# Kernel tuning notes

Measured on AMD Instinct MI355X. Metric: run time of the kernel, lower is better.

## Reference

```python
import jax, jax.numpy as jnp
import numpy as np

EPS = 1e-5

def _layernorm(x, g, b):
    # normalize over last (channel) axis
    mu = jnp.mean(x, axis=-1, keepdims=True)
    var = jnp.var(x, axis=-1, keepdims=True)
    return (x - mu) * jax.lax.rsqrt(var + EPS) * g + b

def _dynamix(xt, wnd, bnd, wnn, bnn):
    # xt: [B, M, N, C]; mixes over the N axis (vectorized form of the per-slice loop)
    B, M, N, C = xt.shape
    d = wnd.shape[1]
    p = xt @ wnd + bnd                       # [B,M,N,d]
    p = p.reshape(B, M, N * d) @ wnn + bnn   # [B,M,N*N]
    p = jax.nn.softmax(p.reshape(B, M, N, N), axis=-1)
    return jnp.einsum('bmij,bmjc->bmic', p, xt)  # [B,M,N,C]

def setup_inputs() -> dict:
    key = jax.random.key(0)
    ks = jax.random.split(key, 10)
    B, C, H, W, d, E = 32, 128, 56, 56, 10, 4
    def n(k, shape, scale=0.02):
        return jax.random.normal(k, shape, jnp.float32) * scale
    return {
        'x': jax.random.normal(ks[0], (B, C, H, W), jnp.float32),
        'ln1_g': jnp.ones((C,), jnp.float32), 'ln1_b': jnp.zeros((C,), jnp.float32),
        'h_wnd': n(ks[1], (C, d)), 'h_bnd': jnp.zeros((d,), jnp.float32),
        'h_wnn': n(ks[2], (W * d, W * W)), 'h_bnn': jnp.zeros((W * W,), jnp.float32),
        'w_wnd': n(ks[3], (C, d)), 'w_bnd': jnp.zeros((d,), jnp.float32),
        'w_wnn': n(ks[4], (H * d, H * H)), 'w_bnn': jnp.zeros((H * H,), jnp.float32),
        'pc_w': n(ks[5], (C, C)), 'pc_b': jnp.zeros((C,), jnp.float32),
        'po_w': n(ks[6], (C, C)), 'po_b': jnp.zeros((C,), jnp.float32),
        'ln2_g': jnp.ones((C,), jnp.float32), 'ln2_b': jnp.zeros((C,), jnp.float32),
        'fc1_w': n(ks[7], (C, E * C)), 'fc1_b': jnp.zeros((E * C,), jnp.float32),
        'fc2_w': n(ks[8], (E * C, C)), 'fc2_b': jnp.zeros((C,), jnp.float32),
    }

def reference(x, ln1_g, ln1_b, h_wnd, h_bnd, h_wnn, h_bnn,
              w_wnd, w_bnd, w_wnn, w_bnn, pc_w, pc_b, po_w, po_b,
              ln2_g, ln2_b, fc1_w, fc1_b, fc2_w, fc2_b):
    # x: [B,C,H,W] -> work channels-last [B,H,W,C]
    xt = jnp.transpose(x, (0, 2, 3, 1))
    # ---- block p1: LN + DynaMixer ----
    u = _layernorm(xt, ln1_g, ln1_b)                 # [B,H,W,C]
    y_h = _dynamix(u, h_wnd, h_bnd, h_wnn, h_bnn)    # mix over W per row
    u_w = jnp.transpose(u, (0, 2, 1, 3))             # [B,W,H,C]
    y_w = _dynamix(u_w, w_wnd, w_bnd, w_wnn, w_bnn)  # mix over H per col
    y_w = jnp.transpose(y_w, (0, 2, 1, 3))           # back to [B,H,W,C]
    y_c = u @ pc_w + pc_b                            # 1x1 conv proj_c
    y = (y_h + y_w + y_c) @ po_w + po_b              # 1x1 conv proj_o
    xt = xt + y                                      # residual (drop_path=0)
    # ---- block p2: LN + MLP ----
    v = _layernorm(xt, ln2_g, ln2_b)
    h = jax.nn.gelu(v @ fc1_w + fc1_b, approximate=False)
    h = h @ fc2_w + fc2_b
    xt = xt + h
    return jnp.transpose(xt, (0, 3, 1, 2))           # [B,C,H,W]
```

## Files before the change

kernel.cpp:

```cpp
#include <hip/hip_runtime.h>
#include <math.h>

#define BB 32
#define CC 128
#define HH 56
#define WW 56
#define HWHW 3136
#define TOK 100352
#define BH 1792
#define NDP 576
#define NNP 3200

typedef __attribute__((ext_vector_type(8))) short bhalf8;
typedef __attribute__((ext_vector_type(4))) float f32x4;
typedef __attribute__((ext_vector_type(4))) unsigned int u32x4;

__device__ inline unsigned short f2bf(float f) {
  unsigned int x = __float_as_uint(f);
  unsigned int r = (x + 0x7FFFu + ((x >> 16) & 1u)) >> 16;
  return (unsigned short)r;
}
__device__ inline float bf2f(unsigned short u) {
  return __uint_as_float(((unsigned int)u) << 16);
}
__device__ inline unsigned int pack2(float a, float b) {
  return (unsigned int)f2bf(a) | ((unsigned int)f2bf(b) << 16);
}
__device__ inline f32x4 MFMA(bhalf8 a, bhalf8 b, f32x4 c) {
  return __builtin_amdgcn_mfma_f32_16x16x32_bf16(a, b, c, 0, 0, 0);
}
template <int CH>
__device__ inline bhalf8 ldsFrag(const unsigned short* base, int row, int chunk) {
  return *reinterpret_cast<const bhalf8*>(base + row * (CH * 8) + ((chunk ^ (row & 7)) * 8));
}
__device__ inline float gelu_f(float x) {
  float x3 = x * x * x;
  float z = 0.7978845608028654f * (x + 0.044715f * x3);
  float e = __expf(2.0f * z);
  float t = 1.0f - 2.0f / (e + 1.0f);
  return 0.5f * x * (1.0f + t);
}

__global__ __launch_bounds__(256) void wcvt_kernel(
    const float* __restrict__ hwnn, const float* __restrict__ wwnn,
    const float* __restrict__ pcw, const float* __restrict__ pow_,
    const float* __restrict__ fc1w, const float* __restrict__ fc2w,
    const float* __restrict__ hwnd, const float* __restrict__ wwnd,
    unsigned short* __restrict__ wnnTh, unsigned short* __restrict__ wnnTw,
    unsigned short* __restrict__ pcT, unsigned short* __restrict__ poT,
    unsigned short* __restrict__ fc1T, unsigned short* __restrict__ fc2T,
    unsigned short* __restrict__ wcatT, u32x4* __restrict__ pdzero) {
  int gt = blockIdx.x * 256 + threadIdx.x;
  int gs = gridDim.x * 256;
  for (int i = gt; i < 258048; i += gs) { u32x4 z = {0, 0, 0, 0}; pdzero[i] = z; }
  for (int i = gt; i < 3200 * 576; i += gs) {
    int k = i / 3200, n = i % 3200;
    float v = (n < 3136 && k < 560) ? hwnn[(size_t)k * 3136 + n] : 0.f;
    wnnTh[(size_t)n * 576 + k] = f2bf(v);
  }
  for (int i = gt; i < 3200 * 576; i += gs) {
    int k = i / 3200, n = i % 3200;
    float v = (n < 3136 && k < 560) ? wwnn[(size_t)k * 3136 + n] : 0.f;
    wnnTw[(size_t)n * 576 + k] = f2bf(v);
  }
  for (int i = gt; i < 128 * 128; i += gs) { int k = i >> 7, n = i & 127; pcT[n * 128 + k] = f2bf(pcw[i]); }
  for (int i = gt; i < 128 * 128; i += gs) { int k = i >> 7, n = i & 127; poT[n * 128 + k] = f2bf(pow_[i]); }
  for (int i = gt; i < 128 * 512; i += gs) { int k = i >> 9, n = i & 511; fc1T[n * 128 + k] = f2bf(fc1w[i]); }
  for (int i = gt; i < 512 * 128; i += gs) { int k = i >> 7, n = i & 127; fc2T[n * 512 + k] = f2bf(fc2w[i]); }
  for (int i = gt; i < 128 * 32; i += gs) {
    int k = i >> 5, n = i & 31;
    float v = n < 10 ? hwnd[k * 10 + n] : (n < 20 ? wwnd[k * 10 + (n - 10)] : 0.f);
    wcatT[n * 128 + k] = f2bf(v);
  }
}

__global__ __launch_bounds__(256) void ln1_kernel(const float* __restrict__ x,
    const float* __restrict__ g, const float* __restrict__ bt,
    unsigned short* __restrict__ ubf, unsigned short* __restrict__ xcl) {
  int bh = blockIdx.x;
  int b = bh / HH, h = bh % HH;
  __shared__ float lds[WW][CC + 1];
  __shared__ float mu[WW], rs[WW];
  const float* xp = x + ((size_t)b * CC) * HWHW + (size_t)h * WW;
  for (int idx = threadIdx.x; idx < CC * WW; idx += 256) {
    int c = idx / WW, w = idx % WW;
    lds[w][c] = xp[(size_t)c * HWHW + w];
  }
  __syncthreads();
  if (threadIdx.x < WW) {
    int w = threadIdx.x;
    float s = 0.f, ss = 0.f;
    for (int c = 0; c < CC; ++c) { float v = lds[w][c]; s += v; ss += v * v; }
    float m = s * (1.0f / CC);
    float var = ss * (1.0f / CC) - m * m;
    mu[w] = m; rs[w] = rsqrtf(var + 1e-5f);
  }
  __syncthreads();
  unsigned short* up = ubf + (size_t)bh * (WW * CC);
  unsigned short* xc = xcl + (size_t)bh * (WW * CC);
  for (int idx = threadIdx.x; idx < WW * CC; idx += 256) {
    int w = idx >> 7, c = idx & 127;
    float v = lds[w][c];
    up[idx] = f2bf((v - mu[w]) * rs[w] * g[c] + bt[c]);
    xc[idx] = f2bf(v);
  }
}

__global__ __launch_bounds__(256) void pd_mfma(const unsigned short* __restrict__ ubf,
    const unsigned short* __restrict__ wcatT, const float* __restrict__ hbnd,
    const float* __restrict__ wbnd, unsigned short* __restrict__ pdh,
    unsigned short* __restrict__ pdw) {
  __shared__ __align__(16) unsigned short sU[64 * 128];
  __shared__ __align__(16) unsigned short sW[32 * 128];
  int tid = threadIdx.x;
  int tok0 = blockIdx.x * 64;
  #pragma unroll
  for (int i = 0; i < 4; ++i) {
    int s = i * 256 + tid; int r = s >> 4, c = s & 15;
    u32x4 v = *reinterpret_cast<const u32x4*>(ubf + (size_t)(tok0 + r) * 128 + c * 8);
    *reinterpret_cast<u32x4*>(sU + r * 128 + ((c ^ (r & 7)) * 8)) = v;
  }
  #pragma unroll
  for (int i = 0; i < 2; ++i) {
    int s = i * 256 + tid; int r = s >> 4, c = s & 15;
    u32x4 v = *reinterpret_cast<const u32x4*>(wcatT + (size_t)r * 128 + c * 8);
    *reinterpret_cast<u32x4*>(sW + r * 128 + ((c ^ (r & 7)) * 8)) = v;
  }
  __syncthreads();
  int wid = tid >> 6, lane = tid & 63, l16 = lane & 15, lk = lane >> 4;
  f32x4 acc[2] = {};
  #pragma unroll
  for (int kk = 0; kk < 4; ++kk) {
    bhalf8 a = ldsFrag<16>(sU, wid * 16 + l16, kk * 4 + lk);
    #pragma unroll
    for (int f = 0; f < 2; ++f) {
      bhalf8 b = ldsFrag<16>(sW, f * 16 + l16, kk * 4 + lk);
      acc[f] = MFMA(a, b, acc[f]);
    }
  }
  #pragma unroll
  for (int f = 0; f < 2; ++f) {
    int n = f * 16 + l16;
    #pragma unroll
    for (int r = 0; r < 4; ++r) {
      int tok = tok0 + wid * 16 + lk * 4 + r;
      float v = acc[f][r];
      if (n < 10) {
        pdh[((size_t)(tok / 56)) * NDP + (size_t)(tok % 56) * 10 + n] = f2bf(v + hbnd[n]);
      } else if (n < 20) {
        int b = tok / HWHW; int rem = tok % HWHW; int hh = rem / 56; int w = rem % 56;
        pdw[((size_t)(b * 56 + w)) * NDP + (size_t)hh * 10 + (n - 10)] = f2bf(v + wbnd[n - 10]);
      }
    }
  }
}

__global__ __launch_bounds__(256) void gemm_logits(
    const unsigned short* __restrict__ A, const unsigned short* __restrict__ BT,
    const float* __restrict__ bias, unsigned short* __restrict__ Cout) {
  __shared__ __align__(16) unsigned short sA[128 * 64];
  __shared__ __align__(16) unsigned short sB[128 * 64];
  int tid = threadIdx.x;
  int row0 = blockIdx.y * 128, col0 = blockIdx.x * 128;
  int wid = tid >> 6, lane = tid & 63;
  int wm = wid >> 1, wn = wid & 1;
  int l16 = lane & 15, lk = lane >> 4;
  f32x4 acc[4][4] = {};
  for (int k0 = 0; k0 < NDP; k0 += 64) {
    #pragma unroll
    for (int i = 0; i < 4; ++i) {
      int s = i * 256 + tid; int r = s >> 3, c = s & 7;
      u32x4 v = *reinterpret_cast<const u32x4*>(A + (size_t)(row0 + r) * NDP + k0 + c * 8);
      *reinterpret_cast<u32x4*>(sA + r * 64 + ((c ^ (r & 7)) * 8)) = v;
    }
    #pragma unroll
    for (int i = 0; i < 4; ++i) {
      int s = i * 256 + tid; int r = s >> 3, c = s & 7;
      u32x4 v = *reinterpret_cast<const u32x4*>(BT + (size_t)(col0 + r) * NDP + k0 + c * 8);
      *reinterpret_cast<u32x4*>(sB + r * 64 + ((c ^ (r & 7)) * 8)) = v;
    }
    __syncthreads();
    bhalf8 af[4][2], bf[4][2];
    #pragma unroll
    for (int f = 0; f < 4; ++f)
      #pragma unroll
      for (int kk = 0; kk < 2; ++kk) {
        af[f][kk] = ldsFrag<8>(sA, wm * 64 + f * 16 + l16, kk * 4 + lk);
        bf[f][kk] = ldsFrag<8>(sB, wn * 64 + f * 16 + l16, kk * 4 + lk);
      }
    #pragma unroll
    for (int i = 0; i < 4; ++i)
      #pragma unroll
      for (int j = 0; j < 4; ++j) {
        acc[i][j] = MFMA(af[i][0], bf[j][0], acc[i][j]);
        acc[i][j] = MFMA(af[i][1], bf[j][1], acc[i][j]);
      }
    __syncthreads();
  }
  #pragma unroll
  for (int i = 0; i < 4; ++i) {
    int rbase = row0 + wm * 64 + i * 16 + lk * 4;
    #pragma unroll
    for (int j = 0; j < 4; ++j) {
      int col = col0 + wn * 64 + j * 16 + l16;
      if (col < HWHW) {
        float bv = bias[col];
        #pragma unroll
        for (int r = 0; r < 4; ++r)
          Cout[(size_t)(rbase + r) * NNP + col] = f2bf(acc[i][j][r] + bv);
      }
    }
  }
}

__global__ __launch_bounds__(256) void softmax56_kernel(unsigned short* __restrict__ ph,
                                                        unsigned short* __restrict__ pw) {
  int wave = (blockIdx.x * 256 + threadIdx.x) >> 6;
  int lane = threadIdx.x & 63;
  if (wave >= 2 * TOK) return;
  unsigned short* buf = wave < TOK ? ph : pw;
  int row = wave < TOK ? wave : wave - TOK;
  int bh = row / 56, i = row % 56;
  unsigned short* p = buf + (size_t)bh * NNP + (size_t)i * 56;
  float xv = lane < WW ? bf2f(p[lane]) : -INFINITY;
  float m = xv;
  for (int o = 32; o > 0; o >>= 1) m = fmaxf(m, __shfl_xor(m, o));
  float e = lane < WW ? __expf(xv - m) : 0.f;
  float s = e;
  for (int o = 32; o > 0; o >>= 1) s += __shfl_xor(s, o);
  if (lane < WW) p[lane] = f2bf(e / s);
}

__global__ __launch_bounds__(256) void mixh_pc(const unsigned short* __restrict__ ph,
    const unsigned short* __restrict__ ubf, const unsigned short* __restrict__ pcT,
    const float* __restrict__ pcb, unsigned short* __restrict__ accm) {
  int bh = blockIdx.x;
  int tok0 = bh * 56;
  __shared__ __align__(16) unsigned short sP[64 * 64];
  __shared__ __align__(16) unsigned short sUn[64 * 128];
  __shared__ __align__(16) unsigned short sUt[128 * 64];
  __shared__ __align__(16) unsigned short pcL[128 * 128];
  int tid = threadIdx.x;
  for (int s = tid; s < 512; s += 256) {
    int r = s >> 3, c = s & 7;
    u32x4 v = {0, 0, 0, 0};
    if (r < 56 && c < 7) v = *reinterpret_cast<const u32x4*>(ph + (size_t)bh * NNP + r * 56 + c * 8);
    *reinterpret_cast<u32x4*>(sP + r * 64 + ((c ^ (r & 7)) * 8)) = v;
  }
  for (int s = tid; s < 1024; s += 256) {
    int r = s >> 4, c = s & 15;
    u32x4 v = {0, 0, 0, 0};
    if (r < 56) v = *reinterpret_cast<const u32x4*>(ubf + (size_t)(tok0 + r) * 128 + c * 8);
    *reinterpret_cast<u32x4*>(sUn + r * 128 + ((c ^ (r & 7)) * 8)) = v;
  }
  for (int s = tid; s < 1024; s += 256) {
    int j = s >> 4, cc = s & 15;
    unsigned short e8[8] = {0, 0, 0, 0, 0, 0, 0, 0};
    if (j < 56)
      *reinterpret_cast<u32x4*>(e8) =
          *reinterpret_cast<const u32x4*>(ubf + (size_t)(tok0 + j) * 128 + cc * 8);
    #pragma unroll
    for (int e = 0; e < 8; ++e) {
      int cf = cc * 8 + e;
      sUt[cf * 64 + (((j >> 3) ^ (cf & 7)) * 8) + (j & 7)] = e8[e];
    }
  }
  for (int s = tid; s < 2048; s += 256) {
    int r = s >> 4, c = s & 15;
    u32x4 v = *reinterpret_cast<const u32x4*>(pcT + (size_t)r * 128 + c * 8);
    *reinterpret_cast<u32x4*>(pcL + r * 128 + ((c ^ (r & 7)) * 8)) = v;
  }
  __syncthreads();
  int lane = tid & 63, l16 = lane & 15, lk = lane >> 4, wn = tid >> 6;
  f32x4 acc[4][2] = {};
  #pragma unroll
  for (int kk = 0; kk < 2; ++kk) {
    bhalf8 a[4], b[2];
    #pragma unroll
    for (int i = 0; i < 4; ++i) a[i] = ldsFrag<8>(sP, i * 16 + l16, kk * 4 + lk);
    #pragma unroll
    for (int j = 0; j < 2; ++j) b[j] = ldsFrag<8>(sUt, wn * 32 + j * 16 + l16, kk * 4 + lk);
    #pragma unroll
    for (int i = 0; i < 4; ++i)
      #pragma unroll
      for (int j = 0; j < 2; ++j) acc[i][j] = MFMA(a[i], b[j], acc[i][j]);
  }
  #pragma unroll
  for (int kk = 0; kk < 4; ++kk) {
    bhalf8 a[4], b[2];
    #pragma unroll
    for (int i = 0; i < 4; ++i) a[i] = ldsFrag<16>(sUn, i * 16 + l16, kk * 4 + lk);
    #pragma unroll
    for (int j = 0; j < 2; ++j) b[j] = ldsFrag<16>(pcL, wn * 32 + j * 16 + l16, kk * 4 + lk);
    #pragma unroll
    for (int i = 0; i < 4; ++i)
      #pragma unroll
      for (int j = 0; j < 2; ++j) acc[i][j] = MFMA(a[i], b[j], acc[i][j]);
  }
  #pragma unroll
  for (int i = 0; i < 4; ++i) {
    int tok = i * 16 + lk * 4;
    #pragma unroll
    for (int j = 0; j < 2; ++j) {
      int c = wn * 32 + j * 16 + l16;
      float bv = pcb[c];
      #pragma unroll
      for (int r = 0; r < 4; ++r)
        if (tok + r < 56)
          accm[(size_t)(tok0 + tok + r) * 128 + c] = f2bf(acc[i][j][r] + bv);
    }
  }
}

__global__ __launch_bounds__(256) void mixw_fin(const unsigned short* __restrict__ pw,
    const unsigned short* __restrict__ ubf, const unsigned short* __restrict__ poT,
    const float* __restrict__ pob, const unsigned short* __restrict__ xcl,
    unsigned short* __restrict__ accXt) {
  int bw = blockIdx.x;
  int bq = bw / 56, w = bw % 56;
  __shared__ __align__(16) unsigned short sP[64 * 64];
  __shared__ __align__(16) unsigned short sUt[128 * 64];
  __shared__ __align__(16) unsigned short sS[64 * 128];
  __shared__ __align__(16) unsigned short poL[128 * 128];
  int tid = threadIdx.x;
  for (int s = tid; s < 512; s += 256) {
    int r = s >> 3, c = s & 7;
    u32x4 v = {0, 0, 0, 0};
    if (r < 56 && c < 7) v = *reinterpret_cast<const u32x4*>(pw + (size_t)bw * NNP + r * 56 + c * 8);
    *reinterpret_cast<u32x4*>(sP + r * 64 + ((c ^ (r & 7)) * 8)) = v;
  }
  for (int s = tid; s < 1024; s += 256) {
    int j = s >> 4, cc = s & 15;
    unsigned short e8[8] = {0, 0, 0, 0, 0, 0, 0, 0};
    if (j < 56)
      *reinterpret_cast<u32x4*>(e8) =
          *reinterpret_cast<const u32x4*>(ubf + ((size_t)bq * HWHW + (size_t)j * 56 + w) * 128 + cc * 8);
    #pragma unroll
    for (int e = 0; e < 8; ++e) {
      int cf = cc * 8 + e;
      sUt[cf * 64 + (((j >> 3) ^ (cf & 7)) * 8) + (j & 7)] = e8[e];
    }
  }
  for (int s = tid; s < 1024; s += 256) {
    int r = s >> 4, c = s & 15;
    u32x4 v = {0, 0, 0, 0};
    if (r < 56) v = *reinterpret_cast<const u32x4*>(accXt + ((size_t)bq * HWHW + (size_t)r * 56 + w) * 128 + c * 8);
    *reinterpret_cast<u32x4*>(sS + r * 128 + ((c ^ (r & 7)) * 8)) = v;
  }
  for (int s = tid; s < 2048; s += 256) {
    int r = s >> 4, c = s & 15;
    u32x4 v = *reinterpret_cast<const u32x4*>(poT + (size_t)r * 128 + c * 8);
    *reinterpret_cast<u32x4*>(poL + r * 128 + ((c ^ (r & 7)) * 8)) = v;
  }
  __syncthreads();
  int lane = tid & 63, l16 = lane & 15, lk = lane >> 4, wn = tid >> 6;
  f32x4 acc1[4][2] = {};
  #pragma unroll
  for (int kk = 0; kk < 2; ++kk) {
    bhalf8 a[4], b[2];
    #pragma unroll
    for (int i = 0; i < 4; ++i) a[i] = ldsFrag<8>(sP, i * 16 + l16, kk * 4 + lk);
    #pragma unroll
    for (int j = 0; j < 2; ++j) b[j] = ldsFrag<8>(sUt, wn * 32 + j * 16 + l16, kk * 4 + lk);
    #pragma unroll
    for (int i = 0; i < 4; ++i)
      #pragma unroll
      for (int j = 0; j < 2; ++j) acc1[i][j] = MFMA(a[i], b[j], acc1[i][j]);
  }
  #pragma unroll
  for (int i = 0; i < 4; ++i) {
    #pragma unroll
    for (int j = 0; j < 2; ++j) {
      int col = wn * 32 + j * 16 + l16;
      #pragma unroll
      for (int r = 0; r < 4; ++r) {
        int row = i * 16 + lk * 4 + r;
        int ad = row * 128 + (((col >> 3) ^ (row & 7)) * 8) + (col & 7);
        sS[ad] = f2bf(bf2f(sS[ad]) + acc1[i][j][r]);
      }
    }
  }
  __syncthreads();
  f32x4 acc2[4][2] = {};
  #pragma unroll
  for (int kk = 0; kk < 4; ++kk) {
    bhalf8 a[4], b[2];
    #pragma unroll
    for (int i = 0; i < 4; ++i) a[i] = ldsFrag<16>(sS, i * 16 + l16, kk * 4 + lk);
    #pragma unroll
    for (int j = 0; j < 2; ++j) b[j] = ldsFrag<16>(poL, wn * 32 + j * 16 + l16, kk * 4 + lk);
    #pragma unroll
    for (int i = 0; i < 4; ++i)
      #pragma unroll
      for (int j = 0; j < 2; ++j) acc2[i][j] = MFMA(a[i], b[j], acc2[i][j]);
  }
  #pragma unroll
  for (int i = 0; i < 4; ++i) {
    #pragma unroll
    for (int j = 0; j < 2; ++j) {
      int c = wn * 32 + j * 16 + l16;
      float bv = pob[c];
      #pragma unroll
      for (int r = 0; r < 4; ++r) {
        int row = i * 16 + lk * 4 + r;
        if (row < 56) {
          size_t t = (size_t)bq * HWHW + (size_t)row * 56 + w;
          float z = acc2[i][j][r] + bv + bf2f(xcl[t * 128 + c]);
          accXt[t * 128 + c] = f2bf(z);
        }
      }
    }
  }
}

__global__ __launch_bounds__(256) void mlp2(const unsigned short* __restrict__ xt2,
    const unsigned short* __restrict__ w1T, const float* __restrict__ b1,
    const unsigned short* __restrict__ w2T, const float* __restrict__ b2,
    const float* __restrict__ g, const float* __restrict__ bt,
    float* __restrict__ out) {
  __shared__ __align__(16) char smem[65536];
  unsigned short* sV = (unsigned short*)smem;
  unsigned short* sW = (unsigned short*)(smem + 16384);
  unsigned short* sH = (unsigned short*)(smem + 49152);
  float* T = (float*)(smem + 16384);
  __shared__ float b1s[512];
  __shared__ float gls[128], bls[128], b2s[128];
  __shared__ float psum[64][4], psq[64][4];
  __shared__ float mus[64], rss[64];
  int tid = threadIdx.x;
  int tok0 = blockIdx.x * 64;
  if (tid < 128) { gls[tid] = g[tid]; bls[tid] = bt[tid]; b2s[tid] = b2[tid]; }
  for (int i = tid; i < 512; i += 256) b1s[i] = b1[i];
  for (int s = tid; s < 1024; s += 256) {
    int r = s >> 4, c = s & 15;
    u32x4 v = *reinterpret_cast<const u32x4*>(xt2 + (size_t)(tok0 + r) * 128 + c * 8);
    #pragma unroll
    for (int e = 0; e < 4; ++e) {
      T[r * 129 + c * 8 + 2 * e]     = bf2f((unsigned short)(v[e] & 0xFFFFu));
      T[r * 129 + c * 8 + 2 * e + 1] = bf2f((unsigned short)(v[e] >> 16));
    }
  }
  __syncthreads();
  {
    int t = tid & 63, q = tid >> 6;
    float s1 = 0.f, s2 = 0.f;
    #pragma unroll 8
    for (int i = 0; i < 32; ++i) { float v = T[t * 129 + q * 32 + i]; s1 += v; s2 += v * v; }
    psum[t][q] = s1; psq[t][q] = s2;
  }
  __syncthreads();
  if (tid < 64) {
    float s1 = psum[tid][0] + psum[tid][1] + psum[tid][2] + psum[tid][3];
    float s2 = psq[tid][0] + psq[tid][1] + psq[tid][2] + psq[tid][3];
    float m = s1 * (1.0f / CC);
    float var = s2 * (1.0f / CC) - m * m;
    mus[tid] = m; rss[tid] = rsqrtf(var + 1e-5f);
  }
  __syncthreads();
  for (int s = tid; s < 1024; s += 256) {
    int r = s >> 4, c = s & 15;
    float m = mus[r], rv = rss[r];
    unsigned int wds[4];
    #pragma unroll
    for (int e = 0; e < 4; ++e) {
      int c0 = c * 8 + 2 * e;
      float v0 = (T[r * 129 + c0]     - m) * rv * gls[c0]     + bls[c0];
      float v1 = (T[r * 129 + c0 + 1] - m) * rv * gls[c0 + 1] + bls[c0 + 1];
      wds[e] = pack2(v0, v1);
    }
    u32x4 v = {wds[0], wds[1], wds[2], wds[3]};
    *reinterpret_cast<u32x4*>(sV + r * 128 + ((c ^ (r & 7)) * 8)) = v;
  }
  __syncthreads();
  int lane = tid & 63, l16 = lane & 15, lk = lane >> 4, wid = tid >> 6;
  int wmA = wid >> 1, wnA = wid & 1;
  int wc = wid >> 1, wt = wid & 1;
  f32x4 acc2[4][2] = {};
  for (int hc = 0; hc < 4; ++hc) {
    for (int s = tid; s < 2048; s += 256) {
      int r = s >> 4, c = s & 15;
      u32x4 v = *reinterpret_cast<const u32x4*>(w1T + (size_t)(hc * 128 + r) * 128 + c * 8);
      *reinterpret_cast<u32x4*>(sW + r * 128 + ((c ^ (r & 7)) * 8)) = v;
    }
    __syncthreads();
    f32x4 acc1[2][4] = {};
    #pragma unroll
    for (int kk = 0; kk < 4; ++kk) {
      bhalf8 a[2], b[4];
      #pragma unroll
      for (int i = 0; i < 2; ++i) a[i] = ldsFrag<16>(sV, wmA * 32 + i * 16 + l16, kk * 4 + lk);
      #pragma unroll
      for (int j = 0; j < 4; ++j) b[j] = ldsFrag<16>(sW, wnA * 64 + j * 16 + l16, kk * 4 + lk);
      #pragma unroll
      for (int i = 0; i < 2; ++i)
        #pragma unroll
        for (int j = 0; j < 4; ++j) acc1[i][j] = MFMA(a[i], b[j], acc1[i][j]);
    }
    #pragma unroll
    for (int i = 0; i < 2; ++i) {
      #pragma unroll
      for (int j = 0; j < 4; ++j) {
        int hid = wnA * 64 + j * 16 + l16;
        float bv = b1s[hc * 128 + hid];
        #pragma unroll
        for (int r = 0; r < 4; ++r) {
          int tok = wmA * 32 + i * 16 + lk * 4 + r;
          float hval = gelu_f(acc1[i][j][r] + bv);
          sH[tok * 128 + (((hid >> 3) ^ (tok & 7)) * 8) + (hid & 7)] = f2bf(hval);
        }
      }
    }
    __syncthreads();
    for (int s = tid; s < 2048; s += 256) {
      int r = s >> 4, c = s & 15;
      u32x4 v = *reinterpret_cast<const u32x4*>(w2T + (size_t)r * 512 + hc * 128 + c * 8);
      *reinterpret_cast<u32x4*>(sW + r * 128 + ((c ^ (r & 7)) * 8)) = v;
    }
    __syncthreads();
    #pragma unroll
    for (int kk = 0; kk < 4; ++kk) {
      bhalf8 a[4], b[2];
      #pragma unroll
      for (int i = 0; i < 4; ++i) a[i] = ldsFrag<16>(sW, wc * 64 + i * 16 + l16, kk * 4 + lk);
      #pragma unroll
      for (int j = 0; j < 2; ++j) b[j] = ldsFrag<16>(sH, wt * 32 + j * 16 + l16, kk * 4 + lk);
      #pragma unroll
      for (int i = 0; i < 4; ++i)
        #pragma unroll
        for (int j = 0; j < 2; ++j) acc2[i][j] = MFMA(a[i], b[j], acc2[i][j]);
    }
    __syncthreads();
  }
  #pragma unroll
  for (int i = 0; i < 4; ++i) {
    #pragma unroll
    for (int j = 0; j < 2; ++j) {
      int tok = wt * 32 + j * 16 + l16;
      #pragma unroll
      for (int r = 0; r < 4; ++r) {
        int c = wc * 64 + i * 16 + lk * 4 + r;
        T[tok * 129 + c] = acc2[i][j][r];
      }
    }
  }
  __syncthreads();
  for (int s = tid; s < 1024; s += 256) {
    int r = s >> 4, c = s & 15;
    u32x4 v = *reinterpret_cast<const u32x4*>(xt2 + (size_t)(tok0 + r) * 128 + c * 8);
    #pragma unroll
    for (int e = 0; e < 4; ++e) {
      int c0 = c * 8 + 2 * e;
      T[r * 129 + c0]     += bf2f((unsigned short)(v[e] & 0xFFFFu)) + b2s[c0];
      T[r * 129 + c0 + 1] += bf2f((unsigned short)(v[e] >> 16))     + b2s[c0 + 1];
    }
  }
  __syncthreads();
  int bq = tok0 / HWHW;
  int pos0 = tok0 % HWHW;
  for (int s = tid; s < 8192; s += 256) {
    int c = s >> 6, t = s & 63;
    out[((size_t)(bq * CC + c)) * HWHW + pos0 + t] = T[t * 129 + c];
  }
}

extern "C" void kernel_launch(void* const* d_in, const int* in_sizes, int n_in,
                              void* d_out, int out_size, void* d_ws, size_t ws_size,
                              hipStream_t stream) {
  const float* x     = (const float*)d_in[0];
  const float* ln1_g = (const float*)d_in[1];
  const float* ln1_b = (const float*)d_in[2];
  const float* h_wnd = (const float*)d_in[3];
  const float* h_bnd = (const float*)d_in[4];
  const float* h_wnn = (const float*)d_in[5];
  const float* h_bnn = (const float*)d_in[6];
  const float* w_wnd = (const float*)d_in[7];
  const float* w_bnd = (const float*)d_in[8];
  const float* w_wnn = (const float*)d_in[9];
  const float* w_bnn = (const float*)d_in[10];
  const float* pc_w  = (const float*)d_in[11];
  const float* pc_b  = (const float*)d_in[12];
  const float* po_w  = (const float*)d_in[13];
  const float* po_b  = (const float*)d_in[14];
  const float* ln2_g = (const float*)d_in[15];
  const float* ln2_b = (const float*)d_in[16];
  const float* fc1_w = (const float*)d_in[17];
  const float* fc1_b = (const float*)d_in[18];
  const float* fc2_w = (const float*)d_in[19];
  const float* fc2_b = (const float*)d_in[20];
  float* out = (float*)d_out;
  char* ws = (char*)d_ws;

  unsigned short* ubf   = (unsigned short*)(ws + 0);
  unsigned short* xcl   = (unsigned short*)(ws + 25690112);
  unsigned short* accXt = (unsigned short*)(ws + 51380224);
  unsigned short* pdh   = (unsigned short*)(ws + 77070336);
  unsigned short* pdw   = (unsigned short*)(ws + 79134720);
  unsigned short* ph    = (unsigned short*)(ws + 81199104);
  unsigned short* pw    = (unsigned short*)(ws + 92667904);
  unsigned short* wnnTh = (unsigned short*)(ws + 104136704);
  unsigned short* wnnTw = (unsigned short*)(ws + 107823104);
  unsigned short* pcT   = (unsigned short*)(ws + 111509504);
  unsigned short* poT   = (unsigned short*)(ws + 111542272);
  unsigned short* fc1T  = (unsigned short*)(ws + 111575040);
  unsigned short* fc2T  = (unsigned short*)(ws + 111706112);
  unsigned short* wcatT = (unsigned short*)(ws + 111837184);

  wcvt_kernel<<<2048, 256, 0, stream>>>(h_wnn, w_wnn, pc_w, po_w, fc1_w, fc2_w,
      h_wnd, w_wnd, wnnTh, wnnTw, pcT, poT, fc1T, fc2T, wcatT, (u32x4*)pdh);
  ln1_kernel<<<BH, 256, 0, stream>>>(x, ln1_g, ln1_b, ubf, xcl);
  pd_mfma<<<TOK / 64, 256, 0, stream>>>(ubf, wcatT, h_bnd, w_bnd, pdh, pdw);
  gemm_logits<<<dim3(NNP / 128, BH / 128), 256, 0, stream>>>(pdh, wnnTh, h_bnn, ph);
  gemm_logits<<<dim3(NNP / 128, BH / 128), 256, 0, stream>>>(pdw, wnnTw, w_bnn, pw);
  softmax56_kernel<<<(2 * TOK) / 4, 256, 0, stream>>>(ph, pw);
  mixh_pc<<<BH, 256, 0, stream>>>(ph, ubf, pcT, pc_b, accXt);
  mixw_fin<<<BB * WW, 256, 0, stream>>>(pw, ubf, poT, po_b, xcl, accXt);
  mlp2<<<TOK / 64, 256, 0, stream>>>(accXt, fc1T, fc1_b, fc2T, fc2_b, ln2_g, ln2_b, out);
}
```

Measured before the change: 332.4 us.

## Split fused MLP into LN2, fc1 and fc2 GEMM kernels with half-batch hidden buffer

Replaces the single fused mlp2 kernel with three kernels: a wave-per-token LayerNorm writing bf16, an fc1 GEMM with 128x128 tiles that applies GELU and writes the hidden activations to a global buffer, and an fc2 GEMM that adds bias and residual and writes NCHW output. The work runs in two halves so the hidden buffer reuses workspace space. The goal is larger, better-shaped MFMA tiles and fewer barriers than the fused per-64-token loop. The cost is an extra round trip through global memory for the 512-wide hidden tensor, plus more launches.

```diff
diff --git a/kernel.cpp b/kernel.cpp
--- a/kernel.cpp
+++ b/kernel.cpp
@@ -7,6 +7,7 @@
 #define WW 56
 #define HWHW 3136
 #define TOK 100352
+#define TOKH 50176
 #define BH 1792
 #define NDP 576
 #define NNP 3200
@@ -413,153 +414,159 @@
   }
 }
 
-__global__ __launch_bounds__(256) void mlp2(const unsigned short* __restrict__ xt2,
-    const unsigned short* __restrict__ w1T, const float* __restrict__ b1,
-    const unsigned short* __restrict__ w2T, const float* __restrict__ b2,
+__global__ __launch_bounds__(256) void ln2_kernel(const unsigned short* __restrict__ xt2,
     const float* __restrict__ g, const float* __restrict__ bt,
-    float* __restrict__ out) {
-  __shared__ __align__(16) char smem[65536];
-  unsigned short* sV = (unsigned short*)smem;
-  unsigned short* sW = (unsigned short*)(smem + 16384);
-  unsigned short* sH = (unsigned short*)(smem + 49152);
-  float* T = (float*)(smem + 16384);
-  __shared__ float b1s[512];
-  __shared__ float gls[128], bls[128], b2s[128];
-  __shared__ float psum[64][4], psq[64][4];
-  __shared__ float mus[64], rss[64];
+    unsigned short* __restrict__ vbf) {
+  int wave = (blockIdx.x * 256 + threadIdx.x) >> 6;
+  int lane = threadIdx.x & 63;
+  if (wave >= TOK) return;
+  const unsigned short* xp = xt2 + (size_t)wave * CC;
+  unsigned int wrd = *reinterpret_cast<const unsigned int*>(xp + lane * 2);
+  float a = bf2f((unsigned short)(wrd & 0xFFFFu));
+  float b2v = bf2f((unsigned short)(wrd >> 16));
+  float s = a + b2v, ss = a * a + b2v * b2v;
+  for (int o = 32; o > 0; o >>= 1) { s += __shfl_xor(s, o); ss += __shfl_xor(ss, o); }
+  float m = s * (1.0f / CC);
+  float var = ss * (1.0f / CC) - m * m;
+  float rv = rsqrtf(var + 1e-5f);
+  int c0 = lane * 2;
+  float n0 = (a - m) * rv * g[c0] + bt[c0];
+  float n1 = (b2v - m) * rv * g[c0 + 1] + bt[c0 + 1];
+  *reinterpret_cast<unsigned int*>(vbf + (size_t)wave * CC + c0) = pack2(n0, n1);
+}
+
+__global__ __launch_bounds__(256) void gemm_fc1(const unsigned short* __restrict__ vbf,
+    const unsigned short* __restrict__ fc1T, const float* __restrict__ b1,
+    unsigned short* __restrict__ hbuf, int tokOff) {
+  __shared__ __align__(16) unsigned short sW[128 * 64];
+  __shared__ __align__(16) unsigned short sV[128 * 64];
+  __shared__ float b1s[128];
   int tid = threadIdx.x;
-  int tok0 = blockIdx.x * 64;
-  if (tid < 128) { gls[tid] = g[tid]; bls[tid] = bt[tid]; b2s[tid] = b2[tid]; }
-  for (int i = tid; i < 512; i += 256) b1s[i] = b1[i];
-  for (int s = tid; s < 1024; s += 256) {
-    int r = s >> 4, c = s & 15;
-    u32x4 v = *reinterpret_cast<const u32x4*>(xt2 + (size_t)(tok0 + r) * 128 + c * 8);
-    #pragma unroll
-    for (int e = 0; e < 4; ++e) {
-      T[r * 129 + c * 8 + 2 * e]     = bf2f((unsigned short)(v[e] & 0xFFFFu));
-      T[r * 129 + c * 8 + 2 * e + 1] = bf2f((unsigned short)(v[e] >> 16));
-    }
+  int hidT = blockIdx.x * 128;
+  int tok0 = blockIdx.y * 128;
+  if (tid < 128) b1s[tid] = b1[hidT + tid];
+  int wid = tid >> 6, lane = tid & 63;
+  int wm = wid >> 1, wn = wid & 1;
+  int l16 = lane & 15, lk = lane >> 4;
+  f32x4 acc[4][4] = {};
+  for (int k0 = 0; k0 < 128; k0 += 64) {
+    #pragma unroll
+    for (int i = 0; i < 4; ++i) {
+      int s = i * 256 + tid; int r = s >> 3, c = s & 7;
+      u32x4 v = *reinterpret_cast<const u32x4*>(fc1T + (size_t)(hidT + r) * 128 + k0 + c * 8);
+      *reinterpret_cast<u32x4*>(sW + r * 64 + ((c ^ (r & 7)) * 8)) = v;
+    }
+    #pragma unroll
+    for (int i = 0; i < 4; ++i) {
+      int s = i * 256 + tid; int r = s >> 3, c = s & 7;
+      u32x4 v = *reinterpret_cast<const u32x4*>(vbf + (size_t)(tokOff + tok0 + r) * 128 + k0 + c * 8);
+      *reinterpret_cast<u32x4*>(sV + r * 64 + ((c ^ (r & 7)) * 8)) = v;
+    }
+    __syncthreads();
+    bhalf8 af[4][2], bf[4][2];
+    #pragma unroll
+    for (int f = 0; f < 4; ++f)
+      #pragma unroll
+      for (int kk = 0; kk < 2; ++kk) {
+        af[f][kk] = ldsFrag<8>(sW, wm * 64 + f * 16 + l16, kk * 4 + lk);
+        bf[f][kk] = ldsFrag<8>(sV, wn * 64 + f * 16 + l16, kk * 4 + lk);
+      }
+    #pragma unroll
+    for (int i = 0; i < 4; ++i)
+      #pragma unroll
+      for (int j = 0; j < 4; ++j) {
+        acc[i][j] = MFMA(af[i][0], bf[j][0], acc[i][j]);
+        acc[i][j] = MFMA(af[i][1], bf[j][1], acc[i][j]);
+      }
+    __syncthreads();
+  }
+  #pragma unroll
+  for (int i = 0; i < 4; ++i) {
+    int hidL = wm * 64 + i * 16 + lk * 4;
+    #pragma unroll
+    for (int j = 0; j < 4; ++j) {
+      int tokL = wn * 64 + j * 16 + l16;
+      float v0 = gelu_f(acc[i][j][0] + b1s[hidL]);
+      float v1 = gelu_f(acc[i][j][1] + b1s[hidL + 1]);
+      float v2 = gelu_f(acc[i][j][2] + b1s[hidL + 2]);
+      float v3 = gelu_f(acc[i][j][3] + b1s[hidL + 3]);
+      unsigned long long pk = (unsigned long long)pack2(v0, v1)
+                            | ((unsigned long long)pack2(v2, v3) << 32);
+      *reinterpret_cast<unsigned long long*>(
+          hbuf + (size_t)(tok0 + tokL) * 512 + hidT + hidL) = pk;
+    }
+  }
+}
+
+__global__ __launch_bounds__(256) void gemm_fc2(const unsigned short* __restrict__ hbuf,
+    const unsigned short* __restrict__ fc2T, const float* __restrict__ b2,
+    const unsigned short* __restrict__ xt2, float* __restrict__ out, int tokOff) {
+  __shared__ __align__(16) unsigned short smem[2][128 * 64];
+  __shared__ float b2s[128];
+  unsigned short* sH = smem[0];
+  unsigned short* sC = smem[1];
+  unsigned short* xtile = &smem[0][0];
+  int tid = threadIdx.x;
+  int tok0 = blockIdx.x * 128;
+  if (tid < 128) b2s[tid] = b2[tid];
+  int wid = tid >> 6, lane = tid & 63;
+  int wm = wid >> 1, wn = wid & 1;
+  int l16 = lane & 15, lk = lane >> 4;
+  f32x4 acc[4][4] = {};
+  for (int k0 = 0; k0 < 512; k0 += 64) {
+    #pragma unroll
+    for (int i = 0; i < 4; ++i) {
+      int s = i * 256 + tid; int r = s >> 3, c = s & 7;
+      u32x4 v = *reinterpret_cast<const u32x4*>(hbuf + (size_t)(tok0 + r) * 512 + k0 + c * 8);
+      *reinterpret_cast<u32x4*>(sH + r * 64 + ((c ^ (r & 7)) * 8)) = v;
+    }
+    #pragma unroll
+    for (int i = 0; i < 4; ++i) {
+      int s = i * 256 + tid; int r = s >> 3, c = s & 7;
+      u32x4 v = *reinterpret_cast<const u32x4*>(fc2T + (size_t)r * 512 + k0 + c * 8);
+      *reinterpret_cast<u32x4*>(sC + r * 64 + ((c ^ (r & 7)) * 8)) = v;
+    }
+    __syncthreads();
+    bhalf8 af[4][2], bf[4][2];
+    #pragma unroll
+    for (int f = 0; f < 4; ++f)
+      #pragma unroll
+      for (int kk = 0; kk < 2; ++kk) {
+        af[f][kk] = ldsFrag<8>(sH, wm * 64 + f * 16 + l16, kk * 4 + lk);
+        bf[f][kk] = ldsFrag<8>(sC, wn * 64 + f * 16 + l16, kk * 4 + lk);
+      }
+    #pragma unroll
+    for (int i = 0; i < 4; ++i)
+      #pragma unroll
+      for (int j = 0; j < 4; ++j) {
+        acc[i][j] = MFMA(af[i][0], bf[j][0], acc[i][j]);
+        acc[i][j] = MFMA(af[i][1], bf[j][1], acc[i][j]);
+      }
+    __syncthreads();
+  }
+  #pragma unroll
+  for (int i = 0; i < 8; ++i) {
+    int s = i * 256 + tid; int r = s >> 4, c = s & 15;
+    u32x4 v = *reinterpret_cast<const u32x4*>(xt2 + (size_t)(tokOff + tok0 + r) * 128 + c * 8);
+    *reinterpret_cast<u32x4*>(xtile + r * 128 + c * 8) = v;
   }
   __syncthreads();
-  {
-    int t = tid & 63, q = tid >> 6;
-    float s1 = 0.f, s2 = 0.f;
-    #pragma unroll 8
-    for (int i = 0; i < 32; ++i) { float v = T[t * 129 + q * 32 + i]; s1 += v; s2 += v * v; }
-    psum[t][q] = s1; psq[t][q] = s2;
-  }
-  __syncthreads();
-  if (tid < 64) {
-    float s1 = psum[tid][0] + psum[tid][1] + psum[tid][2] + psum[tid][3];
-    float s2 = psq[tid][0] + psq[tid][1] + psq[tid][2] + psq[tid][3];
-    float m = s1 * (1.0f / CC);
-    float var = s2 * (1.0f / CC) - m * m;
-    mus[tid] = m; rss[tid] = rsqrtf(var + 1e-5f);
-  }
-  __syncthreads();
-  for (int s = tid; s < 1024; s += 256) {
-    int r = s >> 4, c = s & 15;
-    float m = mus[r], rv = rss[r];
-    unsigned int wds[4];
-    #pragma unroll
-    for (int e = 0; e < 4; ++e) {
-      int c0 = c * 8 + 2 * e;
-      float v0 = (T[r * 129 + c0]     - m) * rv * gls[c0]     + bls[c0];
-      float v1 = (T[r * 129 + c0 + 1] - m) * rv * gls[c0 + 1] + bls[c0 + 1];
-      wds[e] = pack2(v0, v1);
-    }
-    u32x4 v = {wds[0], wds[1], wds[2], wds[3]};
-    *reinterpret_cast<u32x4*>(sV + r * 128 + ((c ^ (r & 7)) * 8)) = v;
-  }
-  __syncthreads();
-  int lane = tid & 63, l16 = lane & 15, lk = lane >> 4, wid = tid >> 6;
-  int wmA = wid >> 1, wnA = wid & 1;
-  int wc = wid >> 1, wt = wid & 1;
-  f32x4 acc2[4][2] = {};
-  for (int hc = 0; hc < 4; ++hc) {
-    for (int s = tid; s < 2048; s += 256) {
-      int r = s >> 4, c = s & 15;
-      u32x4 v = *reinterpret_cast<const u32x4*>(w1T + (size_t)(hc * 128 + r) * 128 + c * 8);
-      *reinterpret_cast<u32x4*>(sW + r * 128 + ((c ^ (r & 7)) * 8)) = v;
-    }
-    __syncthreads();
-    f32x4 acc1[2][4] = {};
-    #pragma unroll
-    for (int kk = 0; kk < 4; ++kk) {
-      bhalf8 a[2], b[4];
-      #pragma unroll
-      for (int i = 0; i < 2; ++i) a[i] = ldsFrag<16>(sV, wmA * 32 + i * 16 + l16, kk * 4 + lk);
-      #pragma unroll
-      for (int j = 0; j < 4; ++j) b[j] = ldsFrag<16>(sW, wnA * 64 + j * 16 + l16, kk * 4 + lk);
-      #pragma unroll
-      for (int i = 0; i < 2; ++i)
-        #pragma unroll
-        for (int j = 0; j < 4; ++j) acc1[i][j] = MFMA(a[i], b[j], acc1[i][j]);
-    }
-    #pragma unroll
-    for (int i = 0; i < 2; ++i) {
-      #pragma unroll
-      for (int j = 0; j < 4; ++j) {
-        int hid = wnA * 64 + j * 16 + l16;
-        float bv = b1s[hc * 128 + hid];
-        #pragma unroll
-        for (int r = 0; r < 4; ++r) {
-          int tok = wmA * 32 + i * 16 + lk * 4 + r;
-          float hval = gelu_f(acc1[i][j][r] + bv);
-          sH[tok * 128 + (((hid >> 3) ^ (tok & 7)) * 8) + (hid & 7)] = f2bf(hval);
-        }
-      }
-    }
-    __syncthreads();
-    for (int s = tid; s < 2048; s += 256) {
-      int r = s >> 4, c = s & 15;
-      u32x4 v = *reinterpret_cast<const u32x4*>(w2T + (size_t)r * 512 + hc * 128 + c * 8);
-      *reinterpret_cast<u32x4*>(sW + r * 128 + ((c ^ (r & 7)) * 8)) = v;
-    }
-    __syncthreads();
-    #pragma unroll
-    for (int kk = 0; kk < 4; ++kk) {
-      bhalf8 a[4], b[2];
-      #pragma unroll
-      for (int i = 0; i < 4; ++i) a[i] = ldsFrag<16>(sW, wc * 64 + i * 16 + l16, kk * 4 + lk);
-      #pragma unroll
-      for (int j = 0; j < 2; ++j) b[j] = ldsFrag<16>(sH, wt * 32 + j * 16 + l16, kk * 4 + lk);
-      #pragma unroll
-      for (int i = 0; i < 4; ++i)
-        #pragma unroll
-        for (int j = 0; j < 2; ++j) acc2[i][j] = MFMA(a[i], b[j], acc2[i][j]);
-    }
-    __syncthreads();
-  }
   #pragma unroll
   for (int i = 0; i < 4; ++i) {
-    #pragma unroll
-    for (int j = 0; j < 2; ++j) {
-      int tok = wt * 32 + j * 16 + l16;
-      #pragma unroll
-      for (int r = 0; r < 4; ++r) {
-        int c = wc * 64 + i * 16 + lk * 4 + r;
-        T[tok * 129 + c] = acc2[i][j][r];
-      }
-    }
-  }
-  __syncthreads();
-  for (int s = tid; s < 1024; s += 256) {
-    int r = s >> 4, c = s & 15;
-    u32x4 v = *reinterpret_cast<const u32x4*>(xt2 + (size_t)(tok0 + r) * 128 + c * 8);
-    #pragma unroll
-    for (int e = 0; e < 4; ++e) {
-      int c0 = c * 8 + 2 * e;
-      T[r * 129 + c0]     += bf2f((unsigned short)(v[e] & 0xFFFFu)) + b2s[c0];
-      T[r * 129 + c0 + 1] += bf2f((unsigned short)(v[e] >> 16))     + b2s[c0 + 1];
-    }
-  }
-  __syncthreads();
-  int bq = tok0 / HWHW;
-  int pos0 = tok0 % HWHW;
-  for (int s = tid; s < 8192; s += 256) {
-    int c = s >> 6, t = s & 63;
-    out[((size_t)(bq * CC + c)) * HWHW + pos0 + t] = T[t * 129 + c];
+    int tokL = wm * 64 + i * 16 + lk * 4;
+    int tokG = tokOff + tok0 + tokL;
+    int bqv = tokG / HWHW;
+    int pos = tokG - bqv * HWHW;
+    #pragma unroll
+    for (int j = 0; j < 4; ++j) {
+      int cL = wn * 64 + j * 16 + l16;
+      float bv = b2s[cL];
+      f32x4 o;
+      #pragma unroll
+      for (int r = 0; r < 4; ++r)
+        o[r] = acc[i][j][r] + bv + bf2f(xtile[(tokL + r) * 128 + cL]);
+      *reinterpret_cast<f32x4*>(out + ((size_t)(bqv * CC + cL)) * HWHW + pos) = o;
+    }
   }
 }
 
@@ -599,11 +606,13 @@
   unsigned short* pw    = (unsigned short*)(ws + 92667904);
   unsigned short* wnnTh = (unsigned short*)(ws + 104136704);
   unsigned short* wnnTw = (unsigned short*)(ws + 107823104);
-  unsigned short* pcT   = (unsigned short*)(ws + 111509504);
-  unsigned short* poT   = (unsigned short*)(ws + 111542272);
-  unsigned short* fc1T  = (unsigned short*)(ws + 111575040);
-  unsigned short* fc2T  = (unsigned short*)(ws + 111706112);
-  unsigned short* wcatT = (unsigned short*)(ws + 111837184);
+  unsigned short* hhalf = (unsigned short*)(ws + 77070336);
+  unsigned short* pcT   = (unsigned short*)(ws + 128450560);
+  unsigned short* poT   = (unsigned short*)(ws + 128483328);
+  unsigned short* fc1T  = (unsigned short*)(ws + 128516096);
+  unsigned short* fc2T  = (unsigned short*)(ws + 128647168);
+  unsigned short* wcatT = (unsigned short*)(ws + 128778240);
+  unsigned short* vbf   = ubf;
 
   wcvt_kernel<<<2048, 256, 0, stream>>>(h_wnn, w_wnn, pc_w, po_w, fc1_w, fc2_w,
       h_wnd, w_wnd, wnnTh, wnnTw, pcT, poT, fc1T, fc2T, wcatT, (u32x4*)pdh);
@@ -614,5 +623,9 @@
   softmax56_kernel<<<(2 * TOK) / 4, 256, 0, stream>>>(ph, pw);
   mixh_pc<<<BH, 256, 0, stream>>>(ph, ubf, pcT, pc_b, accXt);
   mixw_fin<<<BB * WW, 256, 0, stream>>>(pw, ubf, poT, po_b, xcl, accXt);
-  mlp2<<<TOK / 64, 256, 0, stream>>>(accXt, fc1T, fc1_b, fc2T, fc2_b, ln2_g, ln2_b, out);
-}
+  ln2_kernel<<<TOK / 4, 256, 0, stream>>>(accXt, ln2_g, ln2_b, vbf);
+  gemm_fc1<<<dim3(4, TOKH / 128), 256, 0, stream>>>(vbf, fc1T, fc1_b, hhalf, 0);
+  gemm_fc2<<<TOKH / 128, 256, 0, stream>>>(hhalf, fc2T, fc2_b, accXt, out, 0);
+  gemm_fc1<<<dim3(4, TOKH / 128), 256, 0, stream>>>(vbf, fc1T, fc1_b, hhalf, TOKH);
+  gemm_fc2<<<TOKH / 128, 256, 0, stream>>>(hhalf, fc2T, fc2_b, accXt, out, TOKH);
+}
```

Measured after the change: 336.4 us. No clear change (+1.2%).
